# Kernel tuning notes

Hardware: AMD Instinct MI355X
Metric: run time of the kernel (lower is better)

Reference implementation:

```python
import jax, jax.numpy as jnp
import numpy as np

B, L, HS, WS = 4, 5, 32, 32
C = 256            # dim == heads * dim_head
M, D = 8, 32       # heads, dim_head
T, R = 2, 4        # num_types, num_relations
I = M * D          # inner_dim
EPS = 1e-5


def setup_inputs() -> dict:
    key = jax.random.key(0)
    ks = jax.random.split(key, 12)
    w = 0.02
    x = jax.random.normal(ks[0], (B, L, HS, WS, C), dtype=jnp.float32)
    mask = jnp.ones((B, HS, WS, L, L), dtype=jnp.int32)
    prior_encoding = jax.random.randint(ks[1], (B, L, HS, WS, 3), 0, T).astype(jnp.float32)
    return {
        "x": x,
        "mask": mask,
        "prior_encoding": prior_encoding,
        "ln_w": jnp.ones((C,), jnp.float32),
        "ln_b": jnp.zeros((C,), jnp.float32),
        "Wq": jax.random.normal(ks[2], (T, C, I), jnp.float32) * w,
        "bq": jnp.zeros((T, I), jnp.float32),
        "Wk": jax.random.normal(ks[3], (T, C, I), jnp.float32) * w,
        "bk": jnp.zeros((T, I), jnp.float32),
        "Wv": jax.random.normal(ks[4], (T, C, I), jnp.float32) * w,
        "bv": jnp.zeros((T, I), jnp.float32),
        "Wa": jax.random.normal(ks[5], (T, I, C), jnp.float32) * w,
        "ba": jnp.zeros((T, C), jnp.float32),
        "rel_att": jax.random.normal(ks[6], (R, M, D, D), jnp.float32) * w,
        "rel_msg": jax.random.normal(ks[7], (R, M, D, D), jnp.float32) * w,
    }


def _hgt_forward(x, mask, prior_encoding, ln_w, ln_b, Wq, bq, Wk, bk, Wv, bv, Wa, ba, rel_att, rel_msg):
    # pre-LayerNorm over channel dim
    mu = jnp.mean(x, axis=-1, keepdims=True)
    var = jnp.mean(jnp.square(x - mu), axis=-1, keepdims=True)
    xn = (x - mu) * jax.lax.rsqrt(var + EPS) * ln_w + ln_b

    # [B,L,H,W,C] -> [B,H,W,L,C]
    xp = jnp.transpose(xn, (0, 2, 3, 1, 4))
    types = prior_encoding[:, :, 0, 0, 2].astype(jnp.int32)  # [B,L]

    # per-type q/k/v projections via gather of type-indexed weights
    q = jnp.einsum('bhwlc,blci->bhwli', xp, Wq[types]) + bq[types][:, None, None]
    k = jnp.einsum('bhwlc,blci->bhwli', xp, Wk[types]) + bk[types][:, None, None]
    v = jnp.einsum('bhwlc,blci->bhwli', xp, Wv[types]) + bv[types][:, None, None]

    def to_heads(t):  # [B,H,W,L,I] -> [B,M,H,W,L,D]
        return jnp.transpose(t.reshape(B, HS, WS, L, M, D), (0, 4, 1, 2, 3, 5))
    q, k, v = to_heads(q), to_heads(k), to_heads(v)

    # relation-indexed edge weights: e_type = t_i * T + t_j
    e = types[:, :, None] * T + types[:, None, :]              # [B,L,L]
    w_att = jnp.transpose(rel_att[e], (0, 3, 1, 2, 4, 5))      # [B,M,L,L,D,D]
    w_msg = jnp.transpose(rel_msg[e], (0, 3, 1, 2, 4, 5))

    scale = D ** -0.5
    q_w = jnp.einsum('bmhwip,bmijpq->bmhwijq', q, w_att)
    att = jnp.einsum('bmhwijq,bmhwjq->bmhwij', q_w, k) * scale
    att = jnp.where(mask[:, None] == 0, -1e9, att)
    att = jax.nn.softmax(att, axis=-1)

    v_msg = jnp.einsum('bmijpc,bmhwjp->bmhwijc', w_msg, v)
    out = jnp.einsum('bmhwij,bmhwijc->bmhwic', att, v_msg)

    # [B,M,H,W,L,D] -> [B,H,W,L,C]
    out = jnp.transpose(out, (0, 2, 3, 4, 1, 5)).reshape(B, HS, WS, L, I)
    out = jnp.einsum('bhwli,blic->bhwlc', out, Wa[types]) + ba[types][:, None, None]
    # dropout is identity at inference
    return jnp.transpose(out, (0, 3, 1, 2, 4))                 # [B,L,H,W,C]


def reference(x, mask, prior_encoding, ln_w, ln_b, Wq, bq, Wk, bk, Wv, bv, Wa, ba, rel_att, rel_msg):
    return _hgt_forward(x, mask, prior_encoding, ln_w, ln_b, Wq, bq, Wk, bk, Wv, bv, Wa, ba, rel_att, rel_msg)
```

## Files before the change

kernel.cpp:

```cpp
#include <hip/hip_runtime.h>
#include <hip/hip_bf16.h>
#include <math.h>

#define BB 4
#define LL 5
#define HSZ 32
#define WSZ 32
#define PP (HSZ*WSZ)
#define CC 256
#define MM 8
#define DD 32
#define II 256
#define TT 2
#define NTOK (BB*PP*LL*II)
#define TILE_ELEMS 8192
#define SCALE 0.17677669529663687f

typedef short bf16x8 __attribute__((ext_vector_type(8)));
typedef float f32x4 __attribute__((ext_vector_type(4)));

static __device__ __forceinline__ ushort f2bf(float f) {
    unsigned u = __float_as_uint(f);
    unsigned r = (u + 0x7fffu + ((u >> 16) & 1u)) >> 16;
    return (ushort)r;
}
static __device__ __forceinline__ float bf2f(ushort u) {
    return __uint_as_float(((unsigned)u) << 16);
}

__global__ __launch_bounds__(256) void k_fold(
    const float* __restrict__ Wq, const float* __restrict__ Wv,
    const float* __restrict__ Wk, const float* __restrict__ Wa,
    const float* __restrict__ bq, const float* __restrict__ bv,
    const float* __restrict__ rel_att, const float* __restrict__ rel_msg,
    const float* __restrict__ x,
    const float* __restrict__ lnw, const float* __restrict__ lnb,
    ushort* __restrict__ packW, float* __restrict__ bEff,
    ushort* __restrict__ xnPack)
{
    __shared__ float As[1024];
    __shared__ ushort Apack[8192];
    const int blk = blockIdx.x;
    const int tid = threadIdx.x;

    if (blk < 64) {
        const int p  = blk >> 5;
        const int t  = (blk >> 4) & 1;
        const int ts = (blk >> 3) & 1;
        const int m  = blk & 7;
        const float* A = (p == 0)
            ? rel_att + (size_t)((t * 2 + ts) * 8 + m) * 1024
            : rel_msg + (size_t)((ts * 2 + t) * 8 + m) * 1024;
        for (int i = tid; i < 1024; i += 256) As[i] = A[i];
        __syncthreads();

        const float* W = ((p == 0) ? Wq : Wv) + (size_t)t * 65536;
        const int k = tid;
        float wrow[32];
        #pragma unroll
        for (int u = 0; u < 8; ++u)
            *(float4*)&wrow[u * 4] = *(const float4*)&W[k * 256 + m * 32 + u * 4];

        const int slot = (p == 0 ? 0 : 4) + t * 2 + ts;
        ushort* base = packW + (size_t)slot * 65536;
        const int kt = k >> 5, j = k & 7, lq = ((k >> 3) & 3) * 16;
        #pragma unroll
        for (int q = 0; q < 32; ++q) {
            float acc = 0.f;
            #pragma unroll
            for (int pp = 0; pp < 32; ++pp) acc += wrow[pp] * As[pp * 32 + q];
            const int nt = m * 2 + (q >> 4);
            const int lane = lq + (q & 15);
            base[(size_t)((nt * 8 + kt) * 64 + lane) * 8 + j] = f2bf(acc);
        }
        if (tid < 32) {
            const int q = tid;
            const float* bi = ((p == 0) ? bq : bv) + t * 256 + m * 32;
            float acc = 0.f;
            #pragma unroll
            for (int pp = 0; pp < 32; ++pp) acc += bi[pp] * As[pp * 32 + q];
            bEff[(p ? 1024 : 0) + (t * 2 + ts) * 256 + m * 32 + q] = acc;
        }
    } else if (blk < 192) {
        const int idx = blk - 64;
        const int which = idx >> 6;
        const int gi = (idx & 63) * 256 + tid;
        const int t = gi >> 13;
        const int sub = gi & 8191;
        const float* src = ((which == 0) ? Wk : Wa) + (size_t)t * 65536;
        const int slot = (which == 0 ? 8 : 10) + t;
        const int nt = sub >> 9, kt = (sub >> 6) & 7, lane = sub & 63;
        const int k0 = kt * 32 + (lane >> 4) * 8;
        const int n  = nt * 16 + (lane & 15);
        ushort h[8];
        #pragma unroll
        for (int j = 0; j < 8; ++j) h[j] = f2bf(src[(size_t)(k0 + j) * 256 + n]);
        uint4 o;
        o.x = (unsigned)h[0] | ((unsigned)h[1] << 16);
        o.y = (unsigned)h[2] | ((unsigned)h[3] << 16);
        o.z = (unsigned)h[4] | ((unsigned)h[5] << 16);
        o.w = (unsigned)h[6] | ((unsigned)h[7] << 16);
        *(uint4*)(packW + (size_t)slot * 65536 + (size_t)sub * 8) = o;
    } else {
        const int lblk = blk - 192;
        const int bl  = lblk >> 5;
        const int pt  = lblk & 31;
        const int p0  = pt * 32;

        const int r  = tid >> 3;
        const int jj = tid & 7;
        const float* xrow = x + ((size_t)bl * PP + p0 + r) * CC;
        float4 xv[8];
        float s1 = 0.f, s2 = 0.f;
        #pragma unroll
        for (int u = 0; u < 8; ++u) {
            xv[u] = *(const float4*)(xrow + jj * 32 + u * 4);
            s1 += xv[u].x + xv[u].y + xv[u].z + xv[u].w;
            s2 += xv[u].x * xv[u].x + xv[u].y * xv[u].y + xv[u].z * xv[u].z + xv[u].w * xv[u].w;
        }
        s1 += __shfl_xor(s1, 1); s1 += __shfl_xor(s1, 2); s1 += __shfl_xor(s1, 4);
        s2 += __shfl_xor(s2, 1); s2 += __shfl_xor(s2, 2); s2 += __shfl_xor(s2, 4);
        const float mu   = s1 * (1.0f / 256.0f);
        const float var  = s2 * (1.0f / 256.0f) - mu * mu;
        const float rstd = rsqrtf(var + 1e-5f);

        const int mt_r = r >> 4, rm = r & 15;
        #pragma unroll
        for (int u = 0; u < 8; ++u) {
            const int c0 = jj * 32 + u * 4;
            const float4 g  = *(const float4*)(lnw + c0);
            const float4 bt = *(const float4*)(lnb + c0);
            const ushort h0 = f2bf((xv[u].x - mu) * rstd * g.x + bt.x);
            const ushort h1 = f2bf((xv[u].y - mu) * rstd * g.y + bt.y);
            const ushort h2 = f2bf((xv[u].z - mu) * rstd * g.z + bt.z);
            const ushort h3 = f2bf((xv[u].w - mu) * rstd * g.w + bt.w);
            uint2 w2;
            w2.x = (unsigned)h0 | ((unsigned)h1 << 16);
            w2.y = (unsigned)h2 | ((unsigned)h3 << 16);
            const int kt   = c0 >> 5;
            const int lsub = rm + (((c0 >> 3) & 3) << 4);
            const int j0   = c0 & 7;
            *(uint2*)&Apack[(((mt_r * 8 + kt) * 64 + lsub) << 3) + j0] = w2;
        }
        __syncthreads();

        const size_t tbase = (size_t)lblk * TILE_ELEMS;
        #pragma unroll
        for (int u = 0; u < 4; ++u) {
            const int ch = (tid + u * 256) * 8;
            *(uint4*)&xnPack[tbase + ch] = *(const uint4*)&Apack[ch];
        }
    }
}

__global__ __launch_bounds__(256) void k_proj(
    const ushort* __restrict__ xnPack, const float* __restrict__ prior,
    const ushort* __restrict__ packW, const float* __restrict__ bEff,
    const float* __restrict__ bk,
    ushort* __restrict__ qw0, ushort* __restrict__ qw1, ushort* __restrict__ kkO,
    ushort* __restrict__ vm0, ushort* __restrict__ vm1)
{
    __shared__ ushort As[8192];

    const int tid  = threadIdx.x;
    const int blk  = blockIdx.x;
    const int mat  = blk / 640;
    const int rem  = blk - mat * 640;
    const int bl   = rem >> 5;
    const int sub  = rem & 31;
    const int pg   = sub >> 1;
    const int half = sub & 1;
    const int t    = (int)prior[(size_t)bl * (PP * 3) + 2];

    int slot; const float* bias;
    if (mat < 2)       { slot = t * 2 + mat;           bias = bEff + slot * 256; }
    else if (mat == 2) { slot = 8 + t;                 bias = bk + t * 256; }
    else               { slot = 4 + t * 2 + (mat - 3); bias = bEff + 1024 + (t * 2 + (mat - 3)) * 256; }
    ushort* dst = (mat == 0) ? qw0 : (mat == 1) ? qw1 : (mat == 2) ? kkO : (mat == 3) ? vm0 : vm1;

    const int wv = tid >> 6, lane = tid & 63;

    const ushort* Bp = packW + (size_t)slot * 65536;
    bf16x8 bfr[8][2];
    #pragma unroll
    for (int kt = 0; kt < 8; ++kt)
        #pragma unroll
        for (int nn = 0; nn < 2; ++nn) {
            const int ntg = half * 8 + wv * 2 + nn;
            bfr[kt][nn] = *(const bf16x8*)&Bp[(size_t)((ntg * 8 + kt) * 64 + lane) * 8];
        }

    const int cl = lane & 15, rq = lane >> 4;
    const int colA = half * 128 + wv * 32 + cl;
    const int colB = colA + 16;
    const float biasA = bias[colA], biasB = bias[colB];

    #pragma unroll 1
    for (int tl = 0; tl < 2; ++tl) {
        const int pt = pg * 2 + tl;
        const size_t tbase = (size_t)(bl * 32 + pt) * TILE_ELEMS;
        __syncthreads();
        #pragma unroll
        for (int u = 0; u < 4; ++u) {
            const int ch = (tid + u * 256) * 8;
            *(uint4*)&As[ch] = *(const uint4*)&xnPack[tbase + ch];
        }
        __syncthreads();

        f32x4 acc[2][2];
        #pragma unroll
        for (int mt = 0; mt < 2; ++mt)
            #pragma unroll
            for (int nn = 0; nn < 2; ++nn)
                acc[mt][nn] = (f32x4){0.f, 0.f, 0.f, 0.f};

        #pragma unroll
        for (int kt = 0; kt < 8; ++kt) {
            const bf16x8 a0 = *(const bf16x8*)&As[((0 * 8 + kt) * 64 + lane) << 3];
            const bf16x8 a1 = *(const bf16x8*)&As[((1 * 8 + kt) * 64 + lane) << 3];
            acc[0][0] = __builtin_amdgcn_mfma_f32_16x16x32_bf16(a0, bfr[kt][0], acc[0][0], 0, 0, 0);
            acc[0][1] = __builtin_amdgcn_mfma_f32_16x16x32_bf16(a0, bfr[kt][1], acc[0][1], 0, 0, 0);
            acc[1][0] = __builtin_amdgcn_mfma_f32_16x16x32_bf16(a1, bfr[kt][0], acc[1][0], 0, 0, 0);
            acc[1][1] = __builtin_amdgcn_mfma_f32_16x16x32_bf16(a1, bfr[kt][1], acc[1][1], 0, 0, 0);
        }

        const int p0 = pt * 32;
        #pragma unroll
        for (int mt = 0; mt < 2; ++mt) {
            const int row0 = p0 + mt * 16 + rq * 4;
            #pragma unroll
            for (int r2 = 0; r2 < 4; ++r2) {
                const size_t rb = ((size_t)bl * PP + row0 + r2) * II;
                dst[rb + colA] = f2bf(acc[mt][0][r2] + biasA);
                dst[rb + colB] = f2bf(acc[mt][1][r2] + biasB);
            }
        }
    }
}

__global__ __launch_bounds__(256) void k_attn_out(
    const ushort* __restrict__ qw0, const ushort* __restrict__ qw1,
    const ushort* __restrict__ kkI,
    const ushort* __restrict__ vm0, const ushort* __restrict__ vm1,
    const int* __restrict__ mask, const float* __restrict__ prior,
    const ushort* __restrict__ packW, const float* __restrict__ ba,
    float* __restrict__ out)
{
    __shared__ ushort aoS[5 * 16 * 264];
    __shared__ float obufF[16 * 132];

    const int tid  = threadIdx.x;
    const int blk  = blockIdx.x;
    const int half = blk & 1;
    const int gg   = blk >> 1;
    const int b    = gg >> 6;
    const int pg   = gg & 63;
    const int p0   = pg * 16;
    const int wv   = tid >> 6, lane = tid & 63;
    const int c0   = lane * 4;

    int ty[5];
    #pragma unroll
    for (int l = 0; l < 5; ++l)
        ty[l] = (int)prior[(size_t)(b * 5 + l) * (PP * 3) + 2];

    #pragma unroll 1
    for (int it = 0; it < 4; ++it) {
        const int sl   = wv * 4 + it;
        const int pix  = p0 + sl;
        const int site = b * 1024 + pix;
        const int usite = __builtin_amdgcn_readfirstlane(site);

        int mv[5][5];
        #pragma unroll
        for (int i = 0; i < 5; ++i)
            #pragma unroll
            for (int j = 0; j < 5; ++j)
                mv[i][j] = mask[(size_t)usite * 25 + i * 5 + j];

        float qf[2][5][4], kf[5][4];
        #pragma unroll
        for (int l = 0; l < 5; ++l) {
            const size_t base = (((size_t)(b * 5 + l) << 10) + pix) * II + c0;
            const ushort4 q0 = *(const ushort4*)(qw0 + base);
            const ushort4 q1 = *(const ushort4*)(qw1 + base);
            const ushort4 kv = *(const ushort4*)(kkI + base);
            qf[0][l][0] = bf2f(q0.x); qf[0][l][1] = bf2f(q0.y); qf[0][l][2] = bf2f(q0.z); qf[0][l][3] = bf2f(q0.w);
            qf[1][l][0] = bf2f(q1.x); qf[1][l][1] = bf2f(q1.y); qf[1][l][2] = bf2f(q1.z); qf[1][l][3] = bf2f(q1.w);
            kf[l][0]    = bf2f(kv.x); kf[l][1]    = bf2f(kv.y); kf[l][2]    = bf2f(kv.z); kf[l][3]    = bf2f(kv.w);
        }

        float s[5][5];
        #pragma unroll
        for (int j = 0; j < 5; ++j) {
            if (ty[j]) {
                #pragma unroll
                for (int i = 0; i < 5; ++i)
                    s[i][j] = qf[1][i][0] * kf[j][0] + qf[1][i][1] * kf[j][1]
                            + qf[1][i][2] * kf[j][2] + qf[1][i][3] * kf[j][3];
            } else {
                #pragma unroll
                for (int i = 0; i < 5; ++i)
                    s[i][j] = qf[0][i][0] * kf[j][0] + qf[0][i][1] * kf[j][1]
                            + qf[0][i][2] * kf[j][2] + qf[0][i][3] * kf[j][3];
            }
        }
        #pragma unroll
        for (int i = 0; i < 5; ++i)
            #pragma unroll
            for (int j = 0; j < 5; ++j) s[i][j] += __shfl_xor(s[i][j], 1);
        #pragma unroll
        for (int i = 0; i < 5; ++i)
            #pragma unroll
            for (int j = 0; j < 5; ++j) s[i][j] += __shfl_xor(s[i][j], 2);
        #pragma unroll
        for (int i = 0; i < 5; ++i)
            #pragma unroll
            for (int j = 0; j < 5; ++j) s[i][j] += __shfl_xor(s[i][j], 4);

        float vf[2][5][4];
        #pragma unroll
        for (int l = 0; l < 5; ++l) {
            const size_t base = (((size_t)(b * 5 + l) << 10) + pix) * II + c0;
            const ushort4 v0 = *(const ushort4*)(vm0 + base);
            const ushort4 v1 = *(const ushort4*)(vm1 + base);
            vf[0][l][0] = bf2f(v0.x); vf[0][l][1] = bf2f(v0.y); vf[0][l][2] = bf2f(v0.z); vf[0][l][3] = bf2f(v0.w);
            vf[1][l][0] = bf2f(v1.x); vf[1][l][1] = bf2f(v1.y); vf[1][l][2] = bf2f(v1.z); vf[1][l][3] = bf2f(v1.w);
        }

        #pragma unroll
        for (int i = 0; i < 5; ++i) {
            float lg[5];
            #pragma unroll
            for (int j = 0; j < 5; ++j)
                lg[j] = mv[i][j] ? s[i][j] * SCALE : -1e9f;
            const float mx = fmaxf(fmaxf(fmaxf(lg[0], lg[1]), fmaxf(lg[2], lg[3])), lg[4]);
            float ex[5], sum = 0.f;
            #pragma unroll
            for (int j = 0; j < 5; ++j) { ex[j] = __expf(lg[j] - mx); sum += ex[j]; }
            const float rs = 1.0f / sum;
            float o0 = 0.f, o1 = 0.f, o2 = 0.f, o3 = 0.f;
            if (ty[i]) {
                #pragma unroll
                for (int j = 0; j < 5; ++j) {
                    o0 += ex[j] * vf[1][j][0]; o1 += ex[j] * vf[1][j][1];
                    o2 += ex[j] * vf[1][j][2]; o3 += ex[j] * vf[1][j][3];
                }
            } else {
                #pragma unroll
                for (int j = 0; j < 5; ++j) {
                    o0 += ex[j] * vf[0][j][0]; o1 += ex[j] * vf[0][j][1];
                    o2 += ex[j] * vf[0][j][2]; o3 += ex[j] * vf[0][j][3];
                }
            }
            o0 *= rs; o1 *= rs; o2 *= rs; o3 *= rs;
            uint2 w2;
            w2.x = (unsigned)f2bf(o0) | ((unsigned)f2bf(o1) << 16);
            w2.y = (unsigned)f2bf(o2) | ((unsigned)f2bf(o3) << 16);
            *(uint2*)&aoS[(i * 16 + sl) * 264 + c0] = w2;
        }
    }
    __syncthreads();

    const int cl = lane & 15, rq = lane >> 4;
    const int rowA = lane & 15;
    const int ksub = (lane >> 4) * 8;
    const int colL_A = wv * 32 + cl;
    const int colL_B = colL_A + 16;

    #pragma unroll 1
    for (int l = 0; l < 5; ++l) {
        const int t = ty[l];
        const ushort* Bp = packW + (size_t)(10 + t) * 65536;
        bf16x8 bfr[8][2];
        #pragma unroll
        for (int kt = 0; kt < 8; ++kt)
            #pragma unroll
            for (int nn = 0; nn < 2; ++nn) {
                const int ntg = half * 8 + wv * 2 + nn;
                bfr[kt][nn] = *(const bf16x8*)&Bp[(size_t)((ntg * 8 + kt) * 64 + lane) * 8];
            }

        f32x4 acc[2];
        acc[0] = (f32x4){0.f, 0.f, 0.f, 0.f};
        acc[1] = (f32x4){0.f, 0.f, 0.f, 0.f};

        const ushort* aRow = &aoS[(l * 16 + rowA) * 264 + ksub];
        #pragma unroll
        for (int kt = 0; kt < 8; ++kt) {
            const bf16x8 a0 = *(const bf16x8*)(aRow + kt * 32);
            acc[0] = __builtin_amdgcn_mfma_f32_16x16x32_bf16(a0, bfr[kt][0], acc[0], 0, 0, 0);
            acc[1] = __builtin_amdgcn_mfma_f32_16x16x32_bf16(a0, bfr[kt][1], acc[1], 0, 0, 0);
        }

        const float biasA = ba[t * CC + half * 128 + colL_A];
        const float biasB = ba[t * CC + half * 128 + colL_B];

        __syncthreads();
        #pragma unroll
        for (int r2 = 0; r2 < 4; ++r2) {
            obufF[(rq * 4 + r2) * 132 + colL_A] = acc[0][r2] + biasA;
            obufF[(rq * 4 + r2) * 132 + colL_B] = acc[1][r2] + biasB;
        }
        __syncthreads();

        #pragma unroll
        for (int k2 = 0; k2 < 2; ++k2) {
            const int id  = tid + k2 * 256;
            const int row = id >> 5;
            const int ch  = (id & 31) * 4;
            const float4 v4 = *(const float4*)&obufF[row * 132 + ch];
            *(float4*)(out + ((size_t)(b * LL + l) * PP + p0 + row) * CC + half * 128 + ch) = v4;
        }
    }
}

extern "C" void kernel_launch(void* const* d_in, const int* in_sizes, int n_in,
                              void* d_out, int out_size, void* d_ws, size_t ws_size,
                              hipStream_t stream) {
    const float* x       = (const float*)d_in[0];
    const int*   mask    = (const int*)d_in[1];
    const float* prior   = (const float*)d_in[2];
    const float* lnw     = (const float*)d_in[3];
    const float* lnb     = (const float*)d_in[4];
    const float* Wq      = (const float*)d_in[5];
    const float* bq      = (const float*)d_in[6];
    const float* Wk      = (const float*)d_in[7];
    const float* bk      = (const float*)d_in[8];
    const float* Wv      = (const float*)d_in[9];
    const float* bv      = (const float*)d_in[10];
    const float* Wa      = (const float*)d_in[11];
    const float* ba      = (const float*)d_in[12];
    const float* rel_att = (const float*)d_in[13];
    const float* rel_msg = (const float*)d_in[14];
    float* out = (float*)d_out;

    ushort* qw0    = (ushort*)d_ws;
    ushort* qw1    = qw0 + NTOK;
    ushort* kko    = qw1 + NTOK;
    ushort* vm0    = kko + NTOK;
    ushort* vm1    = vm0 + NTOK;
    ushort* xnPack = vm1 + NTOK;
    ushort* packW  = xnPack + NTOK;
    float*  bEff   = (float*)(packW + 12 * 65536);

    hipLaunchKernelGGL(k_fold, dim3(832), dim3(256), 0, stream,
                       Wq, Wv, Wk, Wa, bq, bv, rel_att, rel_msg,
                       x, lnw, lnb, packW, bEff, xnPack);
    hipLaunchKernelGGL(k_proj, dim3(3200), dim3(256), 0, stream,
                       xnPack, prior, packW, bEff, bk, qw0, qw1, kko, vm0, vm1);
    hipLaunchKernelGGL(k_attn_out, dim3(512), dim3(256), 0, stream,
                       qw0, qw1, kko, vm0, vm1, mask, prior, packW, ba, out);
}
```

Measured before the change: 159.1 us.

## Merge channel halves into 512-thread blocks to avoid duplicate attention work

Previously two blocks per pixel group each recomputed the full attention (loading q, k, v for all channels) and then projected only half of the output channels. Now one 512-thread block computes the attention once and splits the output projection across two groups of four waves, writing the full 256-channel row. The global q/k/v loads for a wave's two pixels are also issued up front to increase memory-level parallelism. The trade-off is half as many blocks, larger blocks with more register pressure from the prefetched data, and a bigger shared buffer.

```diff
diff --git a/kernel.cpp b/kernel.cpp
--- a/kernel.cpp
+++ b/kernel.cpp
@@ -238,7 +238,7 @@
     }
 }
 
-__global__ __launch_bounds__(256) void k_attn_out(
+__global__ __launch_bounds__(512) void k_attn_out(
     const ushort* __restrict__ qw0, const ushort* __restrict__ qw1,
     const ushort* __restrict__ kkI,
     const ushort* __restrict__ vm0, const ushort* __restrict__ vm1,
@@ -247,14 +247,12 @@
     float* __restrict__ out)
 {
     __shared__ ushort aoS[5 * 16 * 264];
-    __shared__ float obufF[16 * 132];
+    __shared__ float obufF[16 * 260];
 
     const int tid  = threadIdx.x;
     const int blk  = blockIdx.x;
-    const int half = blk & 1;
-    const int gg   = blk >> 1;
-    const int b    = gg >> 6;
-    const int pg   = gg & 63;
+    const int b    = blk >> 6;
+    const int pg   = blk & 63;
     const int p0   = pg * 16;
     const int wv   = tid >> 6, lane = tid & 63;
     const int c0   = lane * 4;
@@ -264,108 +262,125 @@
     for (int l = 0; l < 5; ++l)
         ty[l] = (int)prior[(size_t)(b * 5 + l) * (PP * 3) + 2];
 
-    #pragma unroll 1
-    for (int it = 0; it < 4; ++it) {
-        const int sl   = wv * 4 + it;
-        const int pix  = p0 + sl;
-        const int site = b * 1024 + pix;
-        const int usite = __builtin_amdgcn_readfirstlane(site);
-
-        int mv[5][5];
-        #pragma unroll
-        for (int i = 0; i < 5; ++i)
-            #pragma unroll
-            for (int j = 0; j < 5; ++j)
-                mv[i][j] = mask[(size_t)usite * 25 + i * 5 + j];
-
-        float qf[2][5][4], kf[5][4];
-        #pragma unroll
-        for (int l = 0; l < 5; ++l) {
-            const size_t base = (((size_t)(b * 5 + l) << 10) + pix) * II + c0;
-            const ushort4 q0 = *(const ushort4*)(qw0 + base);
-            const ushort4 q1 = *(const ushort4*)(qw1 + base);
-            const ushort4 kv = *(const ushort4*)(kkI + base);
-            qf[0][l][0] = bf2f(q0.x); qf[0][l][1] = bf2f(q0.y); qf[0][l][2] = bf2f(q0.z); qf[0][l][3] = bf2f(q0.w);
-            qf[1][l][0] = bf2f(q1.x); qf[1][l][1] = bf2f(q1.y); qf[1][l][2] = bf2f(q1.z); qf[1][l][3] = bf2f(q1.w);
-            kf[l][0]    = bf2f(kv.x); kf[l][1]    = bf2f(kv.y); kf[l][2]    = bf2f(kv.z); kf[l][3]    = bf2f(kv.w);
-        }
-
-        float s[5][5];
-        #pragma unroll
-        for (int j = 0; j < 5; ++j) {
-            if (ty[j]) {
-                #pragma unroll
-                for (int i = 0; i < 5; ++i)
-                    s[i][j] = qf[1][i][0] * kf[j][0] + qf[1][i][1] * kf[j][1]
-                            + qf[1][i][2] * kf[j][2] + qf[1][i][3] * kf[j][3];
-            } else {
-                #pragma unroll
-                for (int i = 0; i < 5; ++i)
-                    s[i][j] = qf[0][i][0] * kf[j][0] + qf[0][i][1] * kf[j][1]
-                            + qf[0][i][2] * kf[j][2] + qf[0][i][3] * kf[j][3];
-            }
-        }
-        #pragma unroll
-        for (int i = 0; i < 5; ++i)
-            #pragma unroll
-            for (int j = 0; j < 5; ++j) s[i][j] += __shfl_xor(s[i][j], 1);
-        #pragma unroll
-        for (int i = 0; i < 5; ++i)
-            #pragma unroll
-            for (int j = 0; j < 5; ++j) s[i][j] += __shfl_xor(s[i][j], 2);
-        #pragma unroll
-        for (int i = 0; i < 5; ++i)
-            #pragma unroll
-            for (int j = 0; j < 5; ++j) s[i][j] += __shfl_xor(s[i][j], 4);
-
-        float vf[2][5][4];
-        #pragma unroll
-        for (int l = 0; l < 5; ++l) {
-            const size_t base = (((size_t)(b * 5 + l) << 10) + pix) * II + c0;
-            const ushort4 v0 = *(const ushort4*)(vm0 + base);
-            const ushort4 v1 = *(const ushort4*)(vm1 + base);
-            vf[0][l][0] = bf2f(v0.x); vf[0][l][1] = bf2f(v0.y); vf[0][l][2] = bf2f(v0.z); vf[0][l][3] = bf2f(v0.w);
-            vf[1][l][0] = bf2f(v1.x); vf[1][l][1] = bf2f(v1.y); vf[1][l][2] = bf2f(v1.z); vf[1][l][3] = bf2f(v1.w);
-        }
-
-        #pragma unroll
-        for (int i = 0; i < 5; ++i) {
-            float lg[5];
-            #pragma unroll
-            for (int j = 0; j < 5; ++j)
-                lg[j] = mv[i][j] ? s[i][j] * SCALE : -1e9f;
-            const float mx = fmaxf(fmaxf(fmaxf(lg[0], lg[1]), fmaxf(lg[2], lg[3])), lg[4]);
-            float ex[5], sum = 0.f;
-            #pragma unroll
-            for (int j = 0; j < 5; ++j) { ex[j] = __expf(lg[j] - mx); sum += ex[j]; }
-            const float rs = 1.0f / sum;
-            float o0 = 0.f, o1 = 0.f, o2 = 0.f, o3 = 0.f;
-            if (ty[i]) {
-                #pragma unroll
-                for (int j = 0; j < 5; ++j) {
-                    o0 += ex[j] * vf[1][j][0]; o1 += ex[j] * vf[1][j][1];
-                    o2 += ex[j] * vf[1][j][2]; o3 += ex[j] * vf[1][j][3];
+    {
+        ushort4 rq0[2][5], rq1[2][5], rkv[2][5], rv0[2][5], rv1[2][5];
+        #pragma unroll
+        for (int it = 0; it < 2; ++it) {
+            const int pix = p0 + wv * 2 + it;
+            #pragma unroll
+            for (int l = 0; l < 5; ++l) {
+                const size_t base = (((size_t)(b * 5 + l) << 10) + pix) * II + c0;
+                rq0[it][l] = *(const ushort4*)(qw0 + base);
+                rq1[it][l] = *(const ushort4*)(qw1 + base);
+                rkv[it][l] = *(const ushort4*)(kkI + base);
+                rv0[it][l] = *(const ushort4*)(vm0 + base);
+                rv1[it][l] = *(const ushort4*)(vm1 + base);
+            }
+        }
+
+        #pragma unroll
+        for (int it = 0; it < 2; ++it) {
+            const int sl   = wv * 2 + it;
+            const int pix  = p0 + sl;
+            const int site = b * 1024 + pix;
+            const int usite = __builtin_amdgcn_readfirstlane(site);
+
+            int mv[5][5];
+            #pragma unroll
+            for (int i = 0; i < 5; ++i)
+                #pragma unroll
+                for (int j = 0; j < 5; ++j)
+                    mv[i][j] = mask[(size_t)usite * 25 + i * 5 + j];
+
+            float qf[2][5][4], kf[5][4];
+            #pragma unroll
+            for (int l = 0; l < 5; ++l) {
+                qf[0][l][0] = bf2f(rq0[it][l].x); qf[0][l][1] = bf2f(rq0[it][l].y);
+                qf[0][l][2] = bf2f(rq0[it][l].z); qf[0][l][3] = bf2f(rq0[it][l].w);
+                qf[1][l][0] = bf2f(rq1[it][l].x); qf[1][l][1] = bf2f(rq1[it][l].y);
+                qf[1][l][2] = bf2f(rq1[it][l].z); qf[1][l][3] = bf2f(rq1[it][l].w);
+                kf[l][0]    = bf2f(rkv[it][l].x); kf[l][1]    = bf2f(rkv[it][l].y);
+                kf[l][2]    = bf2f(rkv[it][l].z); kf[l][3]    = bf2f(rkv[it][l].w);
+            }
+
+            float s[5][5];
+            #pragma unroll
+            for (int j = 0; j < 5; ++j) {
+                if (ty[j]) {
+                    #pragma unroll
+                    for (int i = 0; i < 5; ++i)
+                        s[i][j] = qf[1][i][0] * kf[j][0] + qf[1][i][1] * kf[j][1]
+                                + qf[1][i][2] * kf[j][2] + qf[1][i][3] * kf[j][3];
+                } else {
+                    #pragma unroll
+                    for (int i = 0; i < 5; ++i)
+                        s[i][j] = qf[0][i][0] * kf[j][0] + qf[0][i][1] * kf[j][1]
+                                + qf[0][i][2] * kf[j][2] + qf[0][i][3] * kf[j][3];
                 }
-            } else {
-                #pragma unroll
-                for (int j = 0; j < 5; ++j) {
-                    o0 += ex[j] * vf[0][j][0]; o1 += ex[j] * vf[0][j][1];
-                    o2 += ex[j] * vf[0][j][2]; o3 += ex[j] * vf[0][j][3];
+            }
+            #pragma unroll
+            for (int i = 0; i < 5; ++i)
+                #pragma unroll
+                for (int j = 0; j < 5; ++j) s[i][j] += __shfl_xor(s[i][j], 1);
+            #pragma unroll
+            for (int i = 0; i < 5; ++i)
+                #pragma unroll
+                for (int j = 0; j < 5; ++j) s[i][j] += __shfl_xor(s[i][j], 2);
+            #pragma unroll
+            for (int i = 0; i < 5; ++i)
+                #pragma unroll
+                for (int j = 0; j < 5; ++j) s[i][j] += __shfl_xor(s[i][j], 4);
+
+            float vf[2][5][4];
+            #pragma unroll
+            for (int l = 0; l < 5; ++l) {
+                vf[0][l][0] = bf2f(rv0[it][l].x); vf[0][l][1] = bf2f(rv0[it][l].y);
+                vf[0][l][2] = bf2f(rv0[it][l].z); vf[0][l][3] = bf2f(rv0[it][l].w);
+                vf[1][l][0] = bf2f(rv1[it][l].x); vf[1][l][1] = bf2f(rv1[it][l].y);
+                vf[1][l][2] = bf2f(rv1[it][l].z); vf[1][l][3] = bf2f(rv1[it][l].w);
+            }
+
+            #pragma unroll
+            for (int i = 0; i < 5; ++i) {
+                float lg[5];
+                #pragma unroll
+                for (int j = 0; j < 5; ++j)
+                    lg[j] = mv[i][j] ? s[i][j] * SCALE : -1e9f;
+                const float mx = fmaxf(fmaxf(fmaxf(lg[0], lg[1]), fmaxf(lg[2], lg[3])), lg[4]);
+                float ex[5], sum = 0.f;
+                #pragma unroll
+                for (int j = 0; j < 5; ++j) { ex[j] = __expf(lg[j] - mx); sum += ex[j]; }
+                const float rs = 1.0f / sum;
+                float o0 = 0.f, o1 = 0.f, o2 = 0.f, o3 = 0.f;
+                if (ty[i]) {
+                    #pragma unroll
+                    for (int j = 0; j < 5; ++j) {
+                        o0 += ex[j] * vf[1][j][0]; o1 += ex[j] * vf[1][j][1];
+                        o2 += ex[j] * vf[1][j][2]; o3 += ex[j] * vf[1][j][3];
+                    }
+                } else {
+                    #pragma unroll
+                    for (int j = 0; j < 5; ++j) {
+                        o0 += ex[j] * vf[0][j][0]; o1 += ex[j] * vf[0][j][1];
+                        o2 += ex[j] * vf[0][j][2]; o3 += ex[j] * vf[0][j][3];
+                    }
                 }
-            }
-            o0 *= rs; o1 *= rs; o2 *= rs; o3 *= rs;
-            uint2 w2;
-            w2.x = (unsigned)f2bf(o0) | ((unsigned)f2bf(o1) << 16);
-            w2.y = (unsigned)f2bf(o2) | ((unsigned)f2bf(o3) << 16);
-            *(uint2*)&aoS[(i * 16 + sl) * 264 + c0] = w2;
+                o0 *= rs; o1 *= rs; o2 *= rs; o3 *= rs;
+                uint2 w2;
+                w2.x = (unsigned)f2bf(o0) | ((unsigned)f2bf(o1) << 16);
+                w2.y = (unsigned)f2bf(o2) | ((unsigned)f2bf(o3) << 16);
+                *(uint2*)&aoS[(i * 16 + sl) * 264 + c0] = w2;
+            }
         }
     }
     __syncthreads();
 
+    const int half = wv >> 2;
+    const int wv2  = wv & 3;
     const int cl = lane & 15, rq = lane >> 4;
     const int rowA = lane & 15;
     const int ksub = (lane >> 4) * 8;
-    const int colL_A = wv * 32 + cl;
+    const int colL_A = wv2 * 32 + cl;
     const int colL_B = colL_A + 16;
 
     #pragma unroll 1
@@ -377,7 +392,7 @@
         for (int kt = 0; kt < 8; ++kt)
             #pragma unroll
             for (int nn = 0; nn < 2; ++nn) {
-                const int ntg = half * 8 + wv * 2 + nn;
+                const int ntg = half * 8 + wv2 * 2 + nn;
                 bfr[kt][nn] = *(const bf16x8*)&Bp[(size_t)((ntg * 8 + kt) * 64 + lane) * 8];
             }
 
@@ -399,18 +414,18 @@
         __syncthreads();
         #pragma unroll
         for (int r2 = 0; r2 < 4; ++r2) {
-            obufF[(rq * 4 + r2) * 132 + colL_A] = acc[0][r2] + biasA;
-            obufF[(rq * 4 + r2) * 132 + colL_B] = acc[1][r2] + biasB;
+            obufF[(rq * 4 + r2) * 260 + half * 128 + colL_A] = acc[0][r2] + biasA;
+            obufF[(rq * 4 + r2) * 260 + half * 128 + colL_B] = acc[1][r2] + biasB;
         }
         __syncthreads();
 
         #pragma unroll
         for (int k2 = 0; k2 < 2; ++k2) {
-            const int id  = tid + k2 * 256;
-            const int row = id >> 5;
-            const int ch  = (id & 31) * 4;
-            const float4 v4 = *(const float4*)&obufF[row * 132 + ch];
-            *(float4*)(out + ((size_t)(b * LL + l) * PP + p0 + row) * CC + half * 128 + ch) = v4;
+            const int id  = tid + k2 * 512;
+            const int row = id >> 6;
+            const int ch  = (id & 63) * 4;
+            const float4 v4 = *(const float4*)&obufF[row * 260 + ch];
+            *(float4*)(out + ((size_t)(b * LL + l) * PP + p0 + row) * CC + ch) = v4;
         }
     }
 }
@@ -449,6 +464,6 @@
                        x, lnw, lnb, packW, bEff, xnPack);
     hipLaunchKernelGGL(k_proj, dim3(3200), dim3(256), 0, stream,
                        xnPack, prior, packW, bEff, bk, qw0, qw1, kko, vm0, vm1);
-    hipLaunchKernelGGL(k_attn_out, dim3(512), dim3(256), 0, stream,
+    hipLaunchKernelGGL(k_attn_out, dim3(256), dim3(512), 0, stream,
                        qw0, qw1, kko, vm0, vm1, mask, prior, packW, ba, out);
 }
```

New measurement: 149.2 us, median of 2. 6.2% less time.
